# Optimization experiments

Hardware: AMD Instinct MI355X
Metric: run time of the kernel (lower is better)

Reference implementation:

```python
import jax, jax.numpy as jnp
import numpy as np

NEG_SLOPE = 0.2  # PyG GATConv default negative_slope


def _gat_edge_forward(x, edge_index, edge_attr, W, W_edge, att_src, att_dst, att_edge, bias):
    N = x.shape[0]
    H, C = att_src.shape
    src, dst = edge_index[0], edge_index[1]

    # --- add self loops with edge_attr fill_value='mean' (PyG default) ---
    ones = jnp.ones((edge_attr.shape[0],), dtype=x.dtype)
    cnt = jax.ops.segment_sum(ones, dst, num_segments=N)  # [N]
    attr_sum = jax.ops.segment_sum(edge_attr, dst, num_segments=N)  # [N, edge_dim]
    loop_attr = attr_sum / jnp.maximum(cnt, 1.0)[:, None]  # mean, 0 if no in-edges
    loop_idx = jnp.arange(N, dtype=edge_index.dtype)
    src_all = jnp.concatenate([src, loop_idx])
    dst_all = jnp.concatenate([dst, loop_idx])
    attr_all = jnp.concatenate([edge_attr, loop_attr], axis=0)  # [E+N, edge_dim]

    # --- linear projections ---
    x_l = (x @ W).reshape(N, H, C)  # [N,H,C]; GATConv uses same lin for src/dst
    a_src = jnp.einsum('nhc,hc->nh', x_l, att_src)  # [N,H]
    a_dst = jnp.einsum('nhc,hc->nh', x_l, att_dst)  # [N,H]
    e = (attr_all @ W_edge).reshape(-1, H, C)  # [E+N,H,C]
    a_edge = jnp.einsum('ehc,hc->eh', e, att_edge)  # [E+N,H]

    # --- per-edge attention logits + segment softmax over incoming edges ---
    logits = jax.nn.leaky_relu(a_src[src_all] + a_dst[dst_all] + a_edge, NEG_SLOPE)
    m = jax.ops.segment_max(logits, dst_all, num_segments=N)  # [N,H]
    p = jnp.exp(logits - m[dst_all])
    denom = jax.ops.segment_sum(p, dst_all, num_segments=N)  # [N,H]
    alpha = p / denom[dst_all]  # [E+N,H]

    # --- weighted scatter aggregation ---
    msgs = alpha[:, :, None] * x_l[src_all]  # [E+N,H,C]
    out = jax.ops.segment_sum(msgs, dst_all, num_segments=N)  # [N,H,C]
    return out.reshape(N, H * C) + bias  # concat=True -> [N, H*C]


def setup_inputs() -> dict:
    key = jax.random.key(0)
    ks = jax.random.split(key, 8)
    N, E, DIN, EDIM, H, C = 100000, 1600000, 128, 16, 4, 32
    s = 1.0 / np.sqrt(DIN)
    return {
        'x': jax.random.normal(ks[0], (N, DIN), jnp.float32),
        'edge_index': jax.random.randint(ks[1], (2, E), 0, N, jnp.int64),
        'edge_attr': jax.random.normal(ks[2], (E, EDIM), jnp.float32),
        'W': jax.random.normal(ks[3], (DIN, H * C), jnp.float32) * s,
        'W_edge': jax.random.normal(ks[4], (EDIM, H * C), jnp.float32) * (1.0 / np.sqrt(EDIM)),
        'att_src': jax.random.normal(ks[5], (H, C), jnp.float32) * 0.1,
        'att_dst': jax.random.normal(ks[6], (H, C), jnp.float32) * 0.1,
        'att_edge': jax.random.normal(ks[7], (H, C), jnp.float32) * 0.1,
        'bias': jnp.zeros((H * C,), jnp.float32),
    }


def reference(x, edge_index, edge_attr, W, W_edge, att_src, att_dst, att_edge, bias):
    return _gat_edge_forward(x, edge_index, edge_attr, W, W_edge, att_src, att_dst, att_edge, bias)
```

## Files before the change

### kernel.cpp

```cpp
#include <hip/hip_runtime.h>
#include <hip/hip_fp16.h>
#include <math.h>

#define NEG_SLOPE 0.2f
typedef unsigned short ushort_t;
typedef unsigned int uint_t;

#if defined(__has_builtin)
#if __has_builtin(__builtin_amdgcn_cvt_pk_fp8_f32) && __has_builtin(__builtin_amdgcn_cvt_f32_fp8)
#define HAVE_FP8_CVT 1
#endif
#endif

__device__ __forceinline__ uint_t pack_fp8x4(float a, float b, float c, float d) {
#ifdef HAVE_FP8_CVT
  int v = __builtin_amdgcn_cvt_pk_fp8_f32(a, b, 0, false);
  v = __builtin_amdgcn_cvt_pk_fp8_f32(c, d, v, true);
  return (uint_t)v;
#else
  auto enc = [](float x) -> uint_t {
    uint_t bb = __float_as_uint(x);
    uint_t s = (bb >> 24) & 0x80u;
    int e = (int)((bb >> 23) & 0xffu);
    uint_t m = (bb >> 20) & 7u;
    m += (bb >> 19) & 1u;
    if (m > 7u) { m = 0u; e++; }
    e = e - 127 + 7;
    if (e <= 0) return s;
    if (e > 15) return s | 0x7eu;
    return s | ((uint_t)e << 3) | m;
  };
  return enc(a) | (enc(b) << 8) | (enc(c) << 16) | (enc(d) << 24);
#endif
}

__device__ __forceinline__ float unpack_fp8(uint_t w, int shift) {
#ifdef HAVE_FP8_CVT
  return __builtin_amdgcn_cvt_f32_fp8((int)(w >> shift), 0);
#else
  uint_t b = (w >> shift) & 0xffu;
  uint_t s = (b & 0x80u) << 24;
  uint_t em = b & 0x7fu;
  uint_t f = s | ((em << 20) + (120u << 23));
  return (em == 0u) ? __uint_as_float(s) : __uint_as_float(f);
#endif
}

__global__ void k_prep(const int* __restrict__ ei, int* __restrict__ is64,
                       int* __restrict__ deg, int N,
                       const float* __restrict__ W_edge, const float* __restrict__ att_edge,
                       float* __restrict__ v_edge) {
  int b = blockIdx.x, t = threadIdx.x;
  if (b == 0) {
    __shared__ int any;
    if (t == 0) any = 0;
    __syncthreads();
    if (ei[2 * t + 1] != 0) atomicOr(&any, 1);
    __syncthreads();
    if (t == 0) *is64 = (any == 0) ? 1 : 0;
  } else if (b == 1) {
    if (t < 64) {
      int h = t >> 4, j = t & 15;
      float s = 0.f;
#pragma unroll
      for (int c = 0; c < 32; ++c) s += W_edge[j * 128 + h * 32 + c] * att_edge[h * 32 + c];
      v_edge[t] = s;
    }
  } else {
    int i = (b - 2) * 256 + t;
    if (i < N) deg[i] = 0;
  }
}

__global__ __launch_bounds__(256) void k1_xl(
    const float* __restrict__ x, const float* __restrict__ W,
    const float* __restrict__ att_src, const float* __restrict__ att_dst,
    ushort_t* __restrict__ x_l_h, float* __restrict__ a_src, float* __restrict__ a_dst, int N) {
  __shared__ float Wc[32 * 128];
  __shared__ float Xc[32 * 64];
  const int t = threadIdx.x;
  const int tcol = t & 31;
  const int trow = t >> 5;
  const int row0 = blockIdx.x * 64;
  const int r = t & 63, kq = t >> 6;
  const float4 aw_s = *(const float4*)&att_src[tcol * 4];
  const float4 aw_d = *(const float4*)&att_dst[tcol * 4];
  float acc[8][4];
#pragma unroll
  for (int i = 0; i < 8; ++i) { acc[i][0] = acc[i][1] = acc[i][2] = acc[i][3] = 0.f; }

  for (int kc = 0; kc < 4; ++kc) {
    float4 wreg[4];
#pragma unroll
    for (int q = 0; q < 4; ++q) wreg[q] = *(const float4*)&W[kc * 4096 + (q * 256 + t) * 4];
    float xs8[8];
    int grow = row0 + r;
    if (grow < N) {
      *(float4*)&xs8[0] = *(const float4*)&x[grow * 128 + kc * 32 + kq * 8];
      *(float4*)&xs8[4] = *(const float4*)&x[grow * 128 + kc * 32 + kq * 8 + 4];
    } else {
#pragma unroll
      for (int q = 0; q < 8; ++q) xs8[q] = 0.f;
    }
    __syncthreads();
#pragma unroll
    for (int q = 0; q < 4; ++q) *(float4*)&Wc[(q * 256 + t) * 4] = wreg[q];
#pragma unroll
    for (int q = 0; q < 8; ++q) Xc[(kq * 8 + q) * 64 + r] = xs8[q];
    __syncthreads();
#pragma unroll
    for (int kk = 0; kk < 32; ++kk) {
      float4 wv = *(const float4*)&Wc[kk * 128 + tcol * 4];
      float xr[8];
      *(float4*)&xr[0] = *(const float4*)&Xc[kk * 64 + trow * 8];
      *(float4*)&xr[4] = *(const float4*)&Xc[kk * 64 + trow * 8 + 4];
#pragma unroll
      for (int ri = 0; ri < 8; ++ri) {
        acc[ri][0] += xr[ri] * wv.x;
        acc[ri][1] += xr[ri] * wv.y;
        acc[ri][2] += xr[ri] * wv.z;
        acc[ri][3] += xr[ri] * wv.w;
      }
    }
  }
#pragma unroll
  for (int ri = 0; ri < 8; ++ri) {
    int grow = row0 + trow * 8 + ri;
    float asp = acc[ri][0] * aw_s.x + acc[ri][1] * aw_s.y + acc[ri][2] * aw_s.z + acc[ri][3] * aw_s.w;
    float adp = acc[ri][0] * aw_d.x + acc[ri][1] * aw_d.y + acc[ri][2] * aw_d.z + acc[ri][3] * aw_d.w;
#pragma unroll
    for (int m = 1; m < 8; m <<= 1) { asp += __shfl_xor(asp, m); adp += __shfl_xor(adp, m); }
    if (grow < N) {
      __half2 h0 = __floats2half2_rn(acc[ri][0], acc[ri][1]);
      __half2 h1 = __floats2half2_rn(acc[ri][2], acc[ri][3]);
      uint2 u; u.x = *(uint_t*)&h0; u.y = *(uint_t*)&h1;
      *(uint2*)&x_l_h[(size_t)grow * 128 + tcol * 4] = u;
      if ((tcol & 7) == 0) {
        a_src[grow * 4 + (tcol >> 3)] = asp;
        a_dst[grow * 4 + (tcol >> 3)] = adp;
      }
    }
  }
}

__global__ void k_hist(const int* __restrict__ ei, const int* __restrict__ is64,
                       int* __restrict__ deg, int* __restrict__ rank, int E) {
  int i = blockIdx.x * blockDim.x + threadIdx.x;
  if (i >= E) return;
  int dst = (*is64) ? ei[2 * (E + i)] : ei[E + i];
  rank[i] = atomicAdd(&deg[dst], 1);
}

__global__ void k_scan1(const int* __restrict__ deg, int* __restrict__ bsum, int N) {
  __shared__ int lds[256];
  int b = blockIdx.x, t = threadIdx.x;
  int base = b * 1024 + t * 4;
  int s = 0;
  if (base + 3 < N) {
    int4 v = *(const int4*)&deg[base];
    s = v.x + v.y + v.z + v.w;
  } else {
    for (int q = 0; q < 4; ++q) if (base + q < N) s += deg[base + q];
  }
  lds[t] = s; __syncthreads();
  for (int st = 128; st > 0; st >>= 1) {
    if (t < st) lds[t] += lds[t + st];
    __syncthreads();
  }
  if (t == 0) bsum[b] = lds[0];
}

__global__ void k_scan2(const int* __restrict__ bsum, int* __restrict__ boff, int NB) {
  __shared__ int lds[256];
  int t = threadIdx.x;
  int v = (t < NB) ? bsum[t] : 0;
  lds[t] = v;
  __syncthreads();
  for (int st = 1; st < 256; st <<= 1) {
    int add = (t >= st) ? lds[t - st] : 0;
    __syncthreads();
    lds[t] += add;
    __syncthreads();
  }
  if (t < NB) boff[t] = lds[t] - v;
}

__global__ void k_scan3(const int* __restrict__ deg, const int* __restrict__ boff,
                        int* __restrict__ offs, int N) {
  __shared__ int lds[256];
  int b = blockIdx.x, t = threadIdx.x;
  int base = b * 1024 + t * 4;
  int v[4]; int s = 0;
#pragma unroll
  for (int q = 0; q < 4; ++q) { v[q] = (base + q < N) ? deg[base + q] : 0; s += v[q]; }
  lds[t] = s;
  __syncthreads();
  for (int st = 1; st < 256; st <<= 1) {
    int add = (t >= st) ? lds[t - st] : 0;
    __syncthreads();
    lds[t] += add;
    __syncthreads();
  }
  int run = boff[b] + lds[t] - s;
#pragma unroll
  for (int q = 0; q < 4; ++q) {
    if (base + q < N) offs[base + q] = run;
    run += v[q];
  }
}

__global__ __launch_bounds__(256) void k_scatter(
    const int* __restrict__ ei, const int* __restrict__ is64,
    const int* __restrict__ rank, const int* __restrict__ offs,
    const float* __restrict__ edge_attr, const float* __restrict__ v_edge,
    const float* __restrict__ a_src, const float* __restrict__ a_dst,
    int4* __restrict__ rec, int E) {
  __shared__ float ve[64];
  int t = threadIdx.x;
  if (t < 64) ve[t] = v_edge[t];
  __syncthreads();
  int i = blockIdx.x * 256 + t;
  if (i >= E) return;
  int f = *is64;
  int src = f ? ei[2 * i] : ei[i];
  int dst = f ? ei[2 * (E + i)] : ei[E + i];
  float a16[16];
  *(float4*)&a16[0]  = *(const float4*)&edge_attr[(size_t)i * 16];
  *(float4*)&a16[4]  = *(const float4*)&edge_attr[(size_t)i * 16 + 4];
  *(float4*)&a16[8]  = *(const float4*)&edge_attr[(size_t)i * 16 + 8];
  *(float4*)&a16[12] = *(const float4*)&edge_attr[(size_t)i * 16 + 12];
  float ae[4];
#pragma unroll
  for (int h = 0; h < 4; ++h) {
    float s = 0.f;
#pragma unroll
    for (int j = 0; j < 16; ++j) s += a16[j] * ve[h * 16 + j];
    ae[h] = s;
  }
  float4 as4 = *(const float4*)&a_src[(size_t)src * 4];
  float4 ad4 = *(const float4*)&a_dst[(size_t)dst * 4];
  const float* asp = (const float*)&as4;
  const float* adp = (const float*)&ad4;
  float p[4];
#pragma unroll
  for (int h = 0; h < 4; ++h) {
    float g = asp[h] + adp[h] + ae[h];
    g = fmaxf(g, NEG_SLOPE * g);
    p[h] = __expf(g);
  }
  __half2 p01 = __floats2half2_rn(p[0], p[1]);
  __half2 p23 = __floats2half2_rn(p[2], p[3]);
  uint_t aepk = pack_fp8x4(ae[0], ae[1], ae[2], ae[3]);
  int pos = offs[dst] + rank[i];
  int4 r; r.x = *(int*)&p01; r.y = *(int*)&p23; r.z = src; r.w = (int)aepk;
  rec[pos] = r;
}

__global__ __launch_bounds__(256) void k34_agg(
    const int4* __restrict__ rec, const uint_t* __restrict__ xu,
    const float* __restrict__ a_src, const float* __restrict__ a_dst,
    const int* __restrict__ deg, const int* __restrict__ offs,
    const float* __restrict__ bias, float* __restrict__ out, int N) {
  int lane = threadIdx.x & 63;
  int node = blockIdx.x * 4 + (threadIdx.x >> 6);
  if (node >= N) return;
  int offu = __builtin_amdgcn_readfirstlane(offs[node]);
  int dgu  = __builtin_amdgcn_readfirstlane(deg[node]);
  const int4* rp = rec + offu;
  int h = lane >> 4;
  int hs16 = (h & 1) << 4;
  int hs8  = h << 3;
  float accx = 0.f, accy = 0.f, den = 0.f, sae = 0.f;
  int i = 0;
  for (; i + 4 <= dgu; i += 4) {
    int4 u0 = rp[i], u1 = rp[i + 1], u2 = rp[i + 2], u3 = rp[i + 3];
    int s0 = __builtin_amdgcn_readfirstlane(u0.z);
    int s1 = __builtin_amdgcn_readfirstlane(u1.z);
    int s2 = __builtin_amdgcn_readfirstlane(u2.z);
    int s3 = __builtin_amdgcn_readfirstlane(u3.z);
    uint_t v0 = xu[((size_t)(uint_t)s0 << 6) + lane];
    uint_t v1 = xu[((size_t)(uint_t)s1 << 6) + lane];
    uint_t v2 = xu[((size_t)(uint_t)s2 << 6) + lane];
    uint_t v3 = xu[((size_t)(uint_t)s3 << 6) + lane];
    uint_t w0 = (h & 2) ? (uint_t)u0.y : (uint_t)u0.x;
    uint_t w1 = (h & 2) ? (uint_t)u1.y : (uint_t)u1.x;
    uint_t w2 = (h & 2) ? (uint_t)u2.y : (uint_t)u2.x;
    uint_t w3 = (h & 2) ? (uint_t)u3.y : (uint_t)u3.x;
    float p0 = __half2float(__ushort_as_half((ushort_t)(w0 >> hs16)));
    float p1 = __half2float(__ushort_as_half((ushort_t)(w1 >> hs16)));
    float p2 = __half2float(__ushort_as_half((ushort_t)(w2 >> hs16)));
    float p3 = __half2float(__ushort_as_half((ushort_t)(w3 >> hs16)));
    den += p0 + p1 + p2 + p3;
    sae += unpack_fp8((uint_t)u0.w, hs8) + unpack_fp8((uint_t)u1.w, hs8)
         + unpack_fp8((uint_t)u2.w, hs8) + unpack_fp8((uint_t)u3.w, hs8);
    float2 f0 = __half22float2(*(const __half2*)&v0);
    float2 f1 = __half22float2(*(const __half2*)&v1);
    float2 f2 = __half22float2(*(const __half2*)&v2);
    float2 f3 = __half22float2(*(const __half2*)&v3);
    accx += p0 * f0.x; accy += p0 * f0.y;
    accx += p1 * f1.x; accy += p1 * f1.y;
    accx += p2 * f2.x; accy += p2 * f2.y;
    accx += p3 * f3.x; accy += p3 * f3.y;
  }
  for (; i < dgu; ++i) {
    int4 u = rp[i];
    int s = __builtin_amdgcn_readfirstlane(u.z);
    uint_t v = xu[((size_t)(uint_t)s << 6) + lane];
    uint_t w = (h & 2) ? (uint_t)u.y : (uint_t)u.x;
    float p = __half2float(__ushort_as_half((ushort_t)(w >> hs16)));
    den += p;
    sae += unpack_fp8((uint_t)u.w, hs8);
    float2 fx = __half22float2(*(const __half2*)&v);
    accx += p * fx.x; accy += p * fx.y;
  }
  float ad  = a_dst[(size_t)node * 4 + h];
  float asn = a_src[(size_t)node * 4 + h];
  float inv_cnt = 1.f / (float)(dgu > 0 ? dgu : 1);
  float gl = asn + ad + sae * inv_cnt;
  gl = fmaxf(gl, NEG_SLOPE * gl);
  float pl = __expf(gl);
  float iv = 1.f / (den + pl);
  uint_t vn = xu[((size_t)(uint_t)node << 6) + lane];
  float2 fn = __half22float2(*(const __half2*)&vn);
  float2 b2 = *(const float2*)&bias[2 * lane];
  float2 o;
  o.x = (accx + pl * fn.x) * iv + b2.x;
  o.y = (accy + pl * fn.y) * iv + b2.y;
  *(float2*)&out[(size_t)node * 128 + 2 * lane] = o;
}

extern "C" void kernel_launch(void* const* d_in, const int* in_sizes, int n_in,
                              void* d_out, int out_size, void* d_ws, size_t ws_size,
                              hipStream_t stream) {
  const float* x        = (const float*)d_in[0];
  const int*   ei       = (const int*)  d_in[1];
  const float* eattr    = (const float*)d_in[2];
  const float* W        = (const float*)d_in[3];
  const float* W_edge   = (const float*)d_in[4];
  const float* att_src  = (const float*)d_in[5];
  const float* att_dst  = (const float*)d_in[6];
  const float* att_edge = (const float*)d_in[7];
  const float* bias     = (const float*)d_in[8];
  float* out = (float*)d_out;
  const int N = in_sizes[0] / 128;
  const int E = in_sizes[1] / 2;
  (void)n_in; (void)out_size; (void)ws_size;

  char* base = (char*)d_ws;
  size_t off = 0;
  auto take = [&](size_t bytes) -> void* {
    void* p = base + off;
    off = (off + bytes + 255) & ~(size_t)255;
    return p;
  };
  ushort_t* x_l_h = (ushort_t*)take((size_t)N * 128 * 2);
  float* a_src    = (float*)take((size_t)N * 4 * 4);
  float* a_dst    = (float*)take((size_t)N * 4 * 4);
  float* v_edge   = (float*)take(64 * 4);
  int4*  rec      = (int4*)take((size_t)E * 16);
  int*   deg      = (int*)take((size_t)N * 4);
  int*   offs     = (int*)take((size_t)N * 4);
  int*   rank     = (int*)take((size_t)E * 4);
  int*   bsum     = (int*)take(256 * 4);
  int*   boff     = (int*)take(256 * 4);
  int*   is64     = (int*)take(4);

  const int NB = (N + 1023) / 1024;
  const int nbh = (E + 255) / 256;

  hipLaunchKernelGGL(k_prep, dim3(2 + (N + 255) / 256), dim3(256), 0, stream,
                     ei, is64, deg, N, W_edge, att_edge, v_edge);
  hipLaunchKernelGGL(k_hist, dim3(nbh), dim3(256), 0, stream, ei, is64, deg, rank, E);
  hipLaunchKernelGGL(k1_xl, dim3((N + 63) / 64), dim3(256), 0, stream,
                     x, W, att_src, att_dst, x_l_h, a_src, a_dst, N);
  hipLaunchKernelGGL(k_scan1, dim3(NB), dim3(256), 0, stream, deg, bsum, N);
  hipLaunchKernelGGL(k_scan2, dim3(1), dim3(256), 0, stream, bsum, boff, NB);
  hipLaunchKernelGGL(k_scan3, dim3(NB), dim3(256), 0, stream, deg, boff, offs, N);
  hipLaunchKernelGGL(k_scatter, dim3(nbh), dim3(256), 0, stream,
                     ei, is64, rank, offs, eattr, v_edge, a_src, a_dst, rec, E);
  hipLaunchKernelGGL(k34_agg, dim3((N + 3) / 4), dim3(256), 0, stream,
                     rec, (const uint_t*)x_l_h, a_src, a_dst, deg, offs, bias, out, N);
}
```

Baseline: 296.9 us.

## Replace CSR build with per-node linked lists chased during aggregation

Replaces the degree histogram, three-pass prefix scan and scattered record write with an atomicExch-built linked list per destination node. Edge records are now written in edge order, and the aggregation kernel chases the list, interleaving four nodes per wavefront to hide latency. This removes three scan kernels and the random scatter write. In exchange, aggregation becomes a serial pointer chase with dependent random loads of next[] and rec[], losing the contiguous, coalesced record reads.

```diff
diff --git a/kernel.cpp b/kernel.cpp
--- a/kernel.cpp
+++ b/kernel.cpp
@@ -47,7 +47,7 @@
 }
 
 __global__ void k_prep(const int* __restrict__ ei, int* __restrict__ is64,
-                       int* __restrict__ deg, int N,
+                       int* __restrict__ head, int N,
                        const float* __restrict__ W_edge, const float* __restrict__ att_edge,
                        float* __restrict__ v_edge) {
   int b = blockIdx.x, t = threadIdx.x;
@@ -68,8 +68,16 @@
     }
   } else {
     int i = (b - 2) * 256 + t;
-    if (i < N) deg[i] = 0;
-  }
+    if (i < N) head[i] = -1;
+  }
+}
+
+__global__ void k_build(const int* __restrict__ ei, const int* __restrict__ is64,
+                        int* __restrict__ head, int* __restrict__ next, int E) {
+  int i = blockIdx.x * blockDim.x + threadIdx.x;
+  if (i >= E) return;
+  int dst = (*is64) ? ei[2 * (E + i)] : ei[E + i];
+  next[i] = atomicExch(&head[dst], i);
 }
 
 __global__ __launch_bounds__(256) void k1_xl(
@@ -143,75 +151,8 @@
   }
 }
 
-__global__ void k_hist(const int* __restrict__ ei, const int* __restrict__ is64,
-                       int* __restrict__ deg, int* __restrict__ rank, int E) {
-  int i = blockIdx.x * blockDim.x + threadIdx.x;
-  if (i >= E) return;
-  int dst = (*is64) ? ei[2 * (E + i)] : ei[E + i];
-  rank[i] = atomicAdd(&deg[dst], 1);
-}
-
-__global__ void k_scan1(const int* __restrict__ deg, int* __restrict__ bsum, int N) {
-  __shared__ int lds[256];
-  int b = blockIdx.x, t = threadIdx.x;
-  int base = b * 1024 + t * 4;
-  int s = 0;
-  if (base + 3 < N) {
-    int4 v = *(const int4*)&deg[base];
-    s = v.x + v.y + v.z + v.w;
-  } else {
-    for (int q = 0; q < 4; ++q) if (base + q < N) s += deg[base + q];
-  }
-  lds[t] = s; __syncthreads();
-  for (int st = 128; st > 0; st >>= 1) {
-    if (t < st) lds[t] += lds[t + st];
-    __syncthreads();
-  }
-  if (t == 0) bsum[b] = lds[0];
-}
-
-__global__ void k_scan2(const int* __restrict__ bsum, int* __restrict__ boff, int NB) {
-  __shared__ int lds[256];
-  int t = threadIdx.x;
-  int v = (t < NB) ? bsum[t] : 0;
-  lds[t] = v;
-  __syncthreads();
-  for (int st = 1; st < 256; st <<= 1) {
-    int add = (t >= st) ? lds[t - st] : 0;
-    __syncthreads();
-    lds[t] += add;
-    __syncthreads();
-  }
-  if (t < NB) boff[t] = lds[t] - v;
-}
-
-__global__ void k_scan3(const int* __restrict__ deg, const int* __restrict__ boff,
-                        int* __restrict__ offs, int N) {
-  __shared__ int lds[256];
-  int b = blockIdx.x, t = threadIdx.x;
-  int base = b * 1024 + t * 4;
-  int v[4]; int s = 0;
-#pragma unroll
-  for (int q = 0; q < 4; ++q) { v[q] = (base + q < N) ? deg[base + q] : 0; s += v[q]; }
-  lds[t] = s;
-  __syncthreads();
-  for (int st = 1; st < 256; st <<= 1) {
-    int add = (t >= st) ? lds[t - st] : 0;
-    __syncthreads();
-    lds[t] += add;
-    __syncthreads();
-  }
-  int run = boff[b] + lds[t] - s;
-#pragma unroll
-  for (int q = 0; q < 4; ++q) {
-    if (base + q < N) offs[base + q] = run;
-    run += v[q];
-  }
-}
-
-__global__ __launch_bounds__(256) void k_scatter(
+__global__ __launch_bounds__(256) void k_rec(
     const int* __restrict__ ei, const int* __restrict__ is64,
-    const int* __restrict__ rank, const int* __restrict__ offs,
     const float* __restrict__ edge_attr, const float* __restrict__ v_edge,
     const float* __restrict__ a_src, const float* __restrict__ a_dst,
     int4* __restrict__ rec, int E) {
@@ -251,82 +192,76 @@
   __half2 p01 = __floats2half2_rn(p[0], p[1]);
   __half2 p23 = __floats2half2_rn(p[2], p[3]);
   uint_t aepk = pack_fp8x4(ae[0], ae[1], ae[2], ae[3]);
-  int pos = offs[dst] + rank[i];
   int4 r; r.x = *(int*)&p01; r.y = *(int*)&p23; r.z = src; r.w = (int)aepk;
-  rec[pos] = r;
-}
-
-__global__ __launch_bounds__(256) void k34_agg(
-    const int4* __restrict__ rec, const uint_t* __restrict__ xu,
+  rec[i] = r;
+}
+
+__global__ __launch_bounds__(256) void k34_chase(
+    const int4* __restrict__ rec, const int* __restrict__ next,
+    const int* __restrict__ head, const uint_t* __restrict__ xu,
     const float* __restrict__ a_src, const float* __restrict__ a_dst,
-    const int* __restrict__ deg, const int* __restrict__ offs,
     const float* __restrict__ bias, float* __restrict__ out, int N) {
   int lane = threadIdx.x & 63;
-  int node = blockIdx.x * 4 + (threadIdx.x >> 6);
-  if (node >= N) return;
-  int offu = __builtin_amdgcn_readfirstlane(offs[node]);
-  int dgu  = __builtin_amdgcn_readfirstlane(deg[node]);
-  const int4* rp = rec + offu;
+  int wv = blockIdx.x * 4 + (threadIdx.x >> 6);
+  int n0 = wv * 4;
+  if (n0 >= N) return;
   int h = lane >> 4;
   int hs16 = (h & 1) << 4;
   int hs8  = h << 3;
-  float accx = 0.f, accy = 0.f, den = 0.f, sae = 0.f;
-  int i = 0;
-  for (; i + 4 <= dgu; i += 4) {
-    int4 u0 = rp[i], u1 = rp[i + 1], u2 = rp[i + 2], u3 = rp[i + 3];
-    int s0 = __builtin_amdgcn_readfirstlane(u0.z);
-    int s1 = __builtin_amdgcn_readfirstlane(u1.z);
-    int s2 = __builtin_amdgcn_readfirstlane(u2.z);
-    int s3 = __builtin_amdgcn_readfirstlane(u3.z);
-    uint_t v0 = xu[((size_t)(uint_t)s0 << 6) + lane];
-    uint_t v1 = xu[((size_t)(uint_t)s1 << 6) + lane];
-    uint_t v2 = xu[((size_t)(uint_t)s2 << 6) + lane];
-    uint_t v3 = xu[((size_t)(uint_t)s3 << 6) + lane];
-    uint_t w0 = (h & 2) ? (uint_t)u0.y : (uint_t)u0.x;
-    uint_t w1 = (h & 2) ? (uint_t)u1.y : (uint_t)u1.x;
-    uint_t w2 = (h & 2) ? (uint_t)u2.y : (uint_t)u2.x;
-    uint_t w3 = (h & 2) ? (uint_t)u3.y : (uint_t)u3.x;
-    float p0 = __half2float(__ushort_as_half((ushort_t)(w0 >> hs16)));
-    float p1 = __half2float(__ushort_as_half((ushort_t)(w1 >> hs16)));
-    float p2 = __half2float(__ushort_as_half((ushort_t)(w2 >> hs16)));
-    float p3 = __half2float(__ushort_as_half((ushort_t)(w3 >> hs16)));
-    den += p0 + p1 + p2 + p3;
-    sae += unpack_fp8((uint_t)u0.w, hs8) + unpack_fp8((uint_t)u1.w, hs8)
-         + unpack_fp8((uint_t)u2.w, hs8) + unpack_fp8((uint_t)u3.w, hs8);
-    float2 f0 = __half22float2(*(const __half2*)&v0);
-    float2 f1 = __half22float2(*(const __half2*)&v1);
-    float2 f2 = __half22float2(*(const __half2*)&v2);
-    float2 f3 = __half22float2(*(const __half2*)&v3);
-    accx += p0 * f0.x; accy += p0 * f0.y;
-    accx += p1 * f1.x; accy += p1 * f1.y;
-    accx += p2 * f2.x; accy += p2 * f2.y;
-    accx += p3 * f3.x; accy += p3 * f3.y;
-  }
-  for (; i < dgu; ++i) {
-    int4 u = rp[i];
-    int s = __builtin_amdgcn_readfirstlane(u.z);
-    uint_t v = xu[((size_t)(uint_t)s << 6) + lane];
-    uint_t w = (h & 2) ? (uint_t)u.y : (uint_t)u.x;
-    float p = __half2float(__ushort_as_half((ushort_t)(w >> hs16)));
-    den += p;
-    sae += unpack_fp8((uint_t)u.w, hs8);
-    float2 fx = __half22float2(*(const __half2*)&v);
-    accx += p * fx.x; accy += p * fx.y;
-  }
-  float ad  = a_dst[(size_t)node * 4 + h];
-  float asn = a_src[(size_t)node * 4 + h];
-  float inv_cnt = 1.f / (float)(dgu > 0 ? dgu : 1);
-  float gl = asn + ad + sae * inv_cnt;
-  gl = fmaxf(gl, NEG_SLOPE * gl);
-  float pl = __expf(gl);
-  float iv = 1.f / (den + pl);
-  uint_t vn = xu[((size_t)(uint_t)node << 6) + lane];
-  float2 fn = __half22float2(*(const __half2*)&vn);
-  float2 b2 = *(const float2*)&bias[2 * lane];
-  float2 o;
-  o.x = (accx + pl * fn.x) * iv + b2.x;
-  o.y = (accy + pl * fn.y) * iv + b2.y;
-  *(float2*)&out[(size_t)node * 128 + 2 * lane] = o;
+  float ax0 = 0.f, ay0 = 0.f, dn0 = 0.f, se0 = 0.f;
+  float ax1 = 0.f, ay1 = 0.f, dn1 = 0.f, se1 = 0.f;
+  float ax2 = 0.f, ay2 = 0.f, dn2 = 0.f, se2 = 0.f;
+  float ax3 = 0.f, ay3 = 0.f, dn3 = 0.f, se3 = 0.f;
+  int c0 = 0, c1 = 0, c2 = 0, c3 = 0;
+  int e0 = __builtin_amdgcn_readfirstlane(head[n0]);
+  int e1 = (n0 + 1 < N) ? __builtin_amdgcn_readfirstlane(head[n0 + 1]) : -1;
+  int e2 = (n0 + 2 < N) ? __builtin_amdgcn_readfirstlane(head[n0 + 2]) : -1;
+  int e3 = (n0 + 3 < N) ? __builtin_amdgcn_readfirstlane(head[n0 + 3]) : -1;
+
+  auto step = [&](int& e, float& ax, float& ay, float& dn, float& se, int& ct) {
+    if (e >= 0) {
+      int en = next[e];
+      int4 u = rec[e];
+      uint_t v = xu[((size_t)(uint_t)u.z << 6) + lane];
+      uint_t w = (h & 2) ? (uint_t)u.y : (uint_t)u.x;
+      float p = __half2float(__ushort_as_half((ushort_t)(w >> hs16)));
+      dn += p;
+      se += unpack_fp8((uint_t)u.w, hs8);
+      ct++;
+      float2 fx = __half22float2(*(const __half2*)&v);
+      ax += p * fx.x; ay += p * fx.y;
+      e = __builtin_amdgcn_readfirstlane(en);
+    }
+  };
+
+  while (e0 >= 0 || e1 >= 0 || e2 >= 0 || e3 >= 0) {
+    step(e0, ax0, ay0, dn0, se0, c0);
+    step(e1, ax1, ay1, dn1, se1, c1);
+    step(e2, ax2, ay2, dn2, se2, c2);
+    step(e3, ax3, ay3, dn3, se3, c3);
+  }
+
+  auto fin = [&](int node, float ax, float ay, float dn, float se, int ct) {
+    if (node >= N) return;
+    float ad  = a_dst[(size_t)node * 4 + h];
+    float asn = a_src[(size_t)node * 4 + h];
+    float ic = 1.f / (float)(ct > 0 ? ct : 1);
+    float gl = asn + ad + se * ic;
+    gl = fmaxf(gl, NEG_SLOPE * gl);
+    float pl = __expf(gl);
+    float iv = 1.f / (dn + pl);
+    uint_t vn = xu[((size_t)(uint_t)node << 6) + lane];
+    float2 fn = __half22float2(*(const __half2*)&vn);
+    float2 b2 = *(const float2*)&bias[2 * lane];
+    float2 o;
+    o.x = (ax + pl * fn.x) * iv + b2.x;
+    o.y = (ay + pl * fn.y) * iv + b2.y;
+    *(float2*)&out[(size_t)node * 128 + 2 * lane] = o;
+  };
+  fin(n0, ax0, ay0, dn0, se0, c0);
+  fin(n0 + 1, ax1, ay1, dn1, se1, c1);
+  fin(n0 + 2, ax2, ay2, dn2, se2, c2);
+  fin(n0 + 3, ax3, ay3, dn3, se3, c3);
 }
 
 extern "C" void kernel_launch(void* const* d_in, const int* in_sizes, int n_in,
@@ -358,26 +293,19 @@
   float* a_dst    = (float*)take((size_t)N * 4 * 4);
   float* v_edge   = (float*)take(64 * 4);
   int4*  rec      = (int4*)take((size_t)E * 16);
-  int*   deg      = (int*)take((size_t)N * 4);
-  int*   offs     = (int*)take((size_t)N * 4);
-  int*   rank     = (int*)take((size_t)E * 4);
-  int*   bsum     = (int*)take(256 * 4);
-  int*   boff     = (int*)take(256 * 4);
+  int*   head     = (int*)take((size_t)N * 4);
+  int*   next     = (int*)take((size_t)E * 4);
   int*   is64     = (int*)take(4);
 
-  const int NB = (N + 1023) / 1024;
   const int nbh = (E + 255) / 256;
 
   hipLaunchKernelGGL(k_prep, dim3(2 + (N + 255) / 256), dim3(256), 0, stream,
-                     ei, is64, deg, N, W_edge, att_edge, v_edge);
-  hipLaunchKernelGGL(k_hist, dim3(nbh), dim3(256), 0, stream, ei, is64, deg, rank, E);
+                     ei, is64, head, N, W_edge, att_edge, v_edge);
+  hipLaunchKernelGGL(k_build, dim3(nbh), dim3(256), 0, stream, ei, is64, head, next, E);
   hipLaunchKernelGGL(k1_xl, dim3((N + 63) / 64), dim3(256), 0, stream,
                      x, W, att_src, att_dst, x_l_h, a_src, a_dst, N);
-  hipLaunchKernelGGL(k_scan1, dim3(NB), dim3(256), 0, stream, deg, bsum, N);
-  hipLaunchKernelGGL(k_scan2, dim3(1), dim3(256), 0, stream, bsum, boff, NB);
-  hipLaunchKernelGGL(k_scan3, dim3(NB), dim3(256), 0, stream, deg, boff, offs, N);
-  hipLaunchKernelGGL(k_scatter, dim3(nbh), dim3(256), 0, stream,
-                     ei, is64, rank, offs, eattr, v_edge, a_src, a_dst, rec, E);
-  hipLaunchKernelGGL(k34_agg, dim3((N + 3) / 4), dim3(256), 0, stream,
-                     rec, (const uint_t*)x_l_h, a_src, a_dst, deg, offs, bias, out, N);
-}
+  hipLaunchKernelGGL(k_rec, dim3(nbh), dim3(256), 0, stream,
+                     ei, is64, eattr, v_edge, a_src, a_dst, rec, E);
+  hipLaunchKernelGGL(k34_chase, dim3((N + 15) / 16), dim3(256), 0, stream,
+                     rec, next, head, (const uint_t*)x_l_h, a_src, a_dst, bias, out, N);
+}
```

New measurement: 367.6 us. +23.8%, slower.
